# Performance work log

Hardware: AMD Instinct MI355X
Metric: run time of the kernel (lower is better)

Reference implementation:

```python
import jax, jax.numpy as jnp
import numpy as np

N_NODES = 50000
N_EDGES = 800000
F_IN = 128
HID = 32
H_IN = 4
N_CLS = 47
H_OUT = 4
NEG_SLOPE = 0.2


def _param(k, shape, scale=0.1):
    return jax.random.normal(k, shape, dtype=jnp.float32) * scale


def setup_inputs() -> dict:
    key = jax.random.key(0)
    ks = jax.random.split(key, 14)
    return {
        "x": jax.random.normal(ks[0], (N_NODES, F_IN), dtype=jnp.float32),
        "edge_index": jax.random.randint(ks[1], (2, N_EDGES), 0, N_NODES, dtype=jnp.int64),
        # layer 1: in -> hidden, heads_in, concat
        "W1": _param(ks[2], (F_IN, H_IN * HID)),
        "a1s": _param(ks[3], (H_IN, HID)),
        "a1d": _param(ks[4], (H_IN, HID)),
        "b1": _param(ks[5], (H_IN * HID,)),
        # layer 2: hidden*heads -> hidden, heads_in, concat
        "W2": _param(ks[6], (H_IN * HID, H_IN * HID)),
        "a2s": _param(ks[7], (H_IN, HID)),
        "a2d": _param(ks[8], (H_IN, HID)),
        "b2": _param(ks[9], (H_IN * HID,)),
        # layer 3: hidden*heads -> out, heads_out, mean (concat=False)
        "W3": _param(ks[10], (H_IN * HID, H_OUT * N_CLS)),
        "a3s": _param(ks[11], (H_OUT, N_CLS)),
        "a3d": _param(ks[12], (H_OUT, N_CLS)),
        "b3": _param(ks[13], (N_CLS,)),
    }


def gat_conv(x, W, att_src, att_dst, bias, src, dst, concat):
    """PyG GATConv (self-loops pre-appended in src/dst, eval mode)."""
    n = x.shape[0]
    H, C = att_src.shape
    h = (x @ W).reshape(n, H, C)                      # [N, H, C]
    a_src = jnp.sum(h * att_src[None], axis=-1)       # [N, H]
    a_dst = jnp.sum(h * att_dst[None], axis=-1)       # [N, H]
    alpha = a_src[src] + a_dst[dst]                   # [E, H]
    alpha = jnp.where(alpha >= 0, alpha, NEG_SLOPE * alpha)
    # segment softmax over destination nodes
    m = jax.ops.segment_max(alpha, dst, num_segments=n)  # [N, H]
    e = jnp.exp(alpha - m[dst])
    denom = jax.ops.segment_sum(e, dst, num_segments=n)  # [N, H]
    w = e / denom[dst]                                   # [E, H]
    msg = h[src] * w[:, :, None]                         # [E, H, C]
    out = jax.ops.segment_sum(msg, dst, num_segments=n)  # [N, H, C]
    if concat:
        out = out.reshape(n, H * C)
    else:
        out = out.mean(axis=1)
    return out + bias


def reference(x, edge_index, W1, a1s, a1d, b1, W2, a2s, a2d, b2, W3, a3s, a3d, b3):
    n = x.shape[0]
    loops = jnp.arange(n, dtype=edge_index.dtype)
    src = jnp.concatenate([edge_index[0], loops])
    dst = jnp.concatenate([edge_index[1], loops])
    h = gat_conv(x, W1, a1s, a1d, b1, src, dst, concat=True)
    h = jax.nn.relu(h)
    h = gat_conv(h, W2, a2s, a2d, b2, src, dst, concat=True)
    h = jax.nn.relu(h)
    h = gat_conv(h, W3, a3s, a3d, b3, src, dst, concat=False)
    return jax.nn.log_softmax(h, axis=1)
```

## Files before the change

kernel.cpp:

```cpp
#include <hip/hip_runtime.h>

typedef unsigned short u16;
typedef unsigned int uint32;
typedef __attribute__((ext_vector_type(8))) short short8;
typedef __attribute__((ext_vector_type(4))) float float4v;

#define N_NODES 50000
#define N_EDGES 800000
#define N_TOT   850000
#define NBH 256
#define NB_BKT ((N_NODES + 255) >> 8)
#define NODE_BLOCKS ((N_NODES + 3) / 4)

__device__ __forceinline__ float b2f(u16 u) {
  return __uint_as_float(((unsigned int)u) << 16);
}
__device__ __forceinline__ u16 f2b(float f) {
  unsigned int x = __float_as_uint(f);
  unsigned int r = (x + 0x7fffu + ((x >> 16) & 1u)) >> 16;
  return (u16)r;
}
__device__ __forceinline__ float lo_bf(uint32 g) { return __uint_as_float(g << 16); }
__device__ __forceinline__ float hi_bf(uint32 g) { return __uint_as_float(g & 0xffff0000u); }
__device__ __forceinline__ u16 conv_elem(const void* src, int i, int isf32) {
  if (isf32) return f2b(((const float*)src)[i]);
  return ((const u16*)src)[i];
}
__device__ __forceinline__ float lrelu(float a) { return (a >= 0.f) ? a : 0.2f * a; }
__device__ __forceinline__ int eget(const int* __restrict__ ei, int i, int isI64) {
  return isI64 ? ei[2 * i] : ei[i];
}

__global__ void reorder_all(const u16* __restrict__ x16,
                            const void* W1, const void* W2, const void* W3,
                            const void* a1s, const void* a1d, const void* b1,
                            const void* a2s, const void* a2d, const void* b2,
                            const void* a3s, const void* a3d, const void* b3,
                            int* __restrict__ flags,
                            u16* __restrict__ Wf1, u16* __restrict__ Wf2,
                            u16* __restrict__ Wf3, u16* __restrict__ wt) {
  __shared__ int shF;
  const int tid = threadIdx.x;
  if (tid == 0) shF = 0;
  __syncthreads();
  {
    int emax = 0;
    for (int i = tid; i < 4096; i += 256) {
      int e = (x16[i] >> 7) & 0xFF;
      emax = emax > e ? emax : e;
    }
    if (emax >= 140) atomicOr(&shF, 1);
  }
  __syncthreads();
  const int f32 = shF;
  if (blockIdx.x == 0 && tid == 0) flags[0] = f32;

  int idx = blockIdx.x * 256 + tid;
  if (idx < 57344) {
    const void* W; u16* Wf; int NCOLS, li;
    if (idx < 16384)      { W = W1; Wf = Wf1; NCOLS = 128; li = idx; }
    else if (idx < 32768) { W = W2; Wf = Wf2; NCOLS = 128; li = idx - 16384; }
    else                  { W = W3; Wf = Wf3; NCOLS = 188; li = idx - 32768; }
    int j = li & 7;
    int l = (li >> 3) & 63;
    int c = (li >> 9) & 3;
    int t = li >> 11;
    int k = c * 32 + (l >> 4) * 8 + j;
    int n = t * 16 + (l & 15);
    Wf[li] = (n < NCOLS) ? conv_elem(W, k * NCOLS + n, f32) : (u16)0;
  } else if (idx < 58535) {
    int li = idx - 57344;
    const void* src; int off;
    if (li < 128)       { src = a1s; off = 16384; }
    else if (li < 256)  { src = a1d; off = 16512; li -= 128; }
    else if (li < 384)  { src = b1;  off = 16640; li -= 256; }
    else if (li < 512)  { src = a2s; off = 33152; li -= 384; }
    else if (li < 640)  { src = a2d; off = 33280; li -= 512; }
    else if (li < 768)  { src = b2;  off = 33408; li -= 640; }
    else if (li < 956)  { src = a3s; off = 57600; li -= 768; }
    else if (li < 1144) { src = a3d; off = 57788; li -= 956; }
    else                { src = b3;  off = 57976; li -= 1144; }
    wt[off + li] = conv_elem(src, li, f32);
  }
}


__global__ __launch_bounds__(256) void pack_hist(const int* __restrict__ ei,
                                                 uint32* __restrict__ epack,
                                                 int* __restrict__ cnt) {
  __shared__ int hist[NB_BKT];
  __shared__ int shI;
  const int tid = threadIdx.x;
  if (tid == 0) shI = 0;
  for (int t = tid; t < NB_BKT; t += 256) hist[t] = 0;
  __syncthreads();
  if (ei[2 * tid + 1] != 0) atomicOr(&shI, 1);
  __syncthreads();
  const int i64 = shI ? 0 : 1;
  const int chunk = (N_EDGES + NBH - 1) / NBH;
  const int lo = blockIdx.x * chunk;
  const int hi = min(lo + chunk, N_EDGES);
  for (int e = lo + tid; e < hi; e += 256) {
    int s = eget(ei, e, i64);
    int d = eget(ei, N_EDGES + e, i64);
    epack[e] = ((uint32)d << 16) | (uint32)s;
    atomicAdd(&hist[d >> 8], 1);
  }
  __syncthreads();
  for (int t = tid; t < NB_BKT; t += 256) cnt[t * NBH + blockIdx.x] = hist[t];
}

__global__ __launch_bounds__(256) void scan_cols(int* __restrict__ cnt,
                                                 int* __restrict__ total) {
  __shared__ int ws[4];
  const int bkt = blockIdx.x;
  const int tid = threadIdx.x, lane = tid & 63, wv = tid >> 6;
  int v = cnt[bkt * NBH + tid];
  int incl = v;
#pragma unroll
  for (int off = 1; off < 64; off <<= 1) {
    int t = __shfl_up(incl, off, 64);
    if (lane >= off) incl += t;
  }
  if (lane == 63) ws[wv] = incl;
  __syncthreads();
  if (tid == 0) {
    int s = 0;
#pragma unroll
    for (int w = 0; w < 4; w++) { int t = ws[w]; ws[w] = s; s += t; }
    total[bkt] = s;
  }
  __syncthreads();
  cnt[bkt * NBH + tid] = ws[wv] + incl - v;
}

__global__ __launch_bounds__(256) void scatter_coarse(const uint32* __restrict__ epack,
                                                      const int* __restrict__ cnt,
                                                      const int* __restrict__ btotal,
                                                      uint32* __restrict__ staging) {
  __shared__ int shA[256];
  __shared__ int shW[4];
  const int tid = threadIdx.x, lane = tid & 63, wv = tid >> 6;
  {
    int v = (tid < NB_BKT) ? btotal[tid] : 0;
    int incl = v;
#pragma unroll
    for (int off = 1; off < 64; off <<= 1) {
      int t = __shfl_up(incl, off, 64);
      if (lane >= off) incl += t;
    }
    if (lane == 63) shW[wv] = incl;
    __syncthreads();
    if (tid == 0) {
      int s = 0;
#pragma unroll
      for (int w = 0; w < 4; w++) { int t = shW[w]; shW[w] = s; s += t; }
    }
    __syncthreads();
    shA[tid] = shW[wv] + incl - v;
  }
  __syncthreads();
  for (int t = tid; t < NB_BKT; t += 256) shA[t] += cnt[t * NBH + blockIdx.x];
  __syncthreads();
  const int chunk = (N_EDGES + NBH - 1) / NBH;
  const int lo = blockIdx.x * chunk;
  const int hi = min(lo + chunk, N_EDGES);
  for (int e = lo + tid; e < hi; e += 256) {
    uint32 pk = epack[e];
    int p = atomicAdd(&shA[pk >> 24], 1);
    staging[p] = pk;
  }
}

__global__ __launch_bounds__(256) void build_csr(const uint32* __restrict__ staging,
                                                 const int* __restrict__ btotal,
                                                 int* __restrict__ row_start,
                                                 u16* __restrict__ csr_dst,
                                                 int* __restrict__ csr_src32) {
  __shared__ int shA[256];
  __shared__ int shB[256];
  __shared__ int shW[4];
  const int b = blockIdx.x;
  const int tid = threadIdx.x;
  const int lane = tid & 63, wv = tid >> 6;
  {
    int v = (tid < NB_BKT) ? btotal[tid] : 0;
    int incl = v;
#pragma unroll
    for (int off = 1; off < 64; off <<= 1) {
      int t = __shfl_up(incl, off, 64);
      if (lane >= off) incl += t;
    }
    if (lane == 63) shW[wv] = incl;
    __syncthreads();
    if (tid == 0) {
      int s = 0;
#pragma unroll
      for (int w = 0; w < 4; w++) { int t = shW[w]; shW[w] = s; s += t; }
    }
    __syncthreads();
    shA[tid] = shW[wv] + incl - v;
  }
  __syncthreads();
  const int lo = shA[b];
  const int hi = lo + btotal[b];
  __syncthreads();
  shA[tid] = 0;
  __syncthreads();
  for (int i = lo + tid; i < hi; i += 256)
    atomicAdd(&shA[(staging[i] >> 16) & 255], 1);
  __syncthreads();
  int v = shA[tid];
  int incl = v;
#pragma unroll
  for (int off = 1; off < 64; off <<= 1) {
    int t = __shfl_up(incl, off, 64);
    if (lane >= off) incl += t;
  }
  if (lane == 63) shW[wv] = incl;
  __syncthreads();
  if (tid == 0) {
    int s = 0;
#pragma unroll
    for (int w = 0; w < 4; w++) { int t = shW[w]; shW[w] = s; s += t; }
  }
  __syncthreads();
  int excl = shW[wv] + incl - v;
  const int n = (b << 8) + tid;
  if (n < N_NODES) {
    int rs = lo + (b << 8) + excl + tid;
    row_start[n] = rs;
    csr_src32[rs] = n;
    u16 g16 = (u16)n;
    for (int k = 0; k <= v; k++) csr_dst[rs + k] = g16;
    shB[tid] = rs + 1;
  }
  if (b == NB_BKT - 1 && tid == 0) row_start[N_NODES] = N_TOT;
  __syncthreads();
  for (int i = lo + tid; i < hi; i += 256) {
    uint32 pk = staging[i];
    int p = atomicAdd(&shB[(pk >> 16) & 255], 1);
    csr_src32[p] = (int)(pk & 0xffffu);
  }
}

template <int NT, int NCOLS, int STRIDE, bool FUSE_A, bool CMAJOR, bool FUSE3, bool RAWX>
__global__ __launch_bounds__(256) void gemm_mfma(const void* __restrict__ X,
                                                 const u16* __restrict__ Wf,
                                                 const u16* __restrict__ attS,
                                                 const u16* __restrict__ attD,
                                                 const int* __restrict__ flags,
                                                 u16* __restrict__ H,
                                                 float* __restrict__ a_s,
                                                 float* __restrict__ a_d, int M) {
  const int wid = __builtin_amdgcn_readfirstlane(threadIdx.x >> 6);
  const int lane = threadIdx.x & 63;
  const int row0 = (blockIdx.x * 4 + wid) * 16;
  if (row0 >= M) return;
  const int qr = lane >> 4;
  const int ln = lane & 15;

  float4v acc[NT];
#pragma unroll
  for (int t = 0; t < NT; t++) acc[t] = (float4v){0.f, 0.f, 0.f, 0.f};

  const short8* Wf8 = (const short8*)Wf;
  const size_t aoff = (size_t)(row0 + ln) * 128 + qr * 8;
  int f32m = 0;
  if constexpr (RAWX) f32m = flags[0];

#pragma unroll
  for (int c = 0; c < 4; c++) {
    short8 afrag;
    if constexpr (RAWX) {
      if (f32m) {
        const float* ap = (const float*)X + aoff + c * 32;
        float4 lo = ((const float4*)ap)[0];
        float4 hi = ((const float4*)ap)[1];
        afrag[0] = (short)f2b(lo.x); afrag[1] = (short)f2b(lo.y);
        afrag[2] = (short)f2b(lo.z); afrag[3] = (short)f2b(lo.w);
        afrag[4] = (short)f2b(hi.x); afrag[5] = (short)f2b(hi.y);
        afrag[6] = (short)f2b(hi.z); afrag[7] = (short)f2b(hi.w);
      } else {
        afrag = *(const short8*)((const u16*)X + aoff + c * 32);
      }
    } else {
      afrag = *(const short8*)((const u16*)X + aoff + c * 32);
    }
#pragma unroll
    for (int t = 0; t < NT; t++) {
      short8 bfrag = Wf8[(t * 4 + c) * 64 + lane];
      acc[t] = __builtin_amdgcn_mfma_f32_16x16x32_bf16(afrag, bfrag, acc[t], 0, 0, 0);
    }
  }

#pragma unroll
  for (int t = 0; t < NT; t++) {
    int col = t * 16 + ln;
    if (col < NCOLS) {
      int off;
      if constexpr (CMAJOR) {
        int h = (col >= 141) ? 3 : (col >= 94) ? 2 : (col >= 47) ? 1 : 0;
        int c = col - h * 47;
        off = c * 4 + h;
      } else {
        off = col;
      }
#pragma unroll
      for (int i = 0; i < 4; i++) {
        H[(size_t)(row0 + qr * 4 + i) * STRIDE + off] = f2b(acc[t][i]);
      }
    } else {
      if constexpr (CMAJOR) {
#pragma unroll
        for (int i = 0; i < 4; i++) {
          H[(size_t)(row0 + qr * 4 + i) * STRIDE + col] = (u16)0x3F80;
        }
      }
    }
  }

  if constexpr (FUSE_A) {
    float aSf[NT], aDf[NT];
#pragma unroll
    for (int t = 0; t < NT; t++) {
      aSf[t] = b2f(attS[t * 16 + ln]);
      aDf[t] = b2f(attD[t * 16 + ln]);
    }
#pragma unroll
    for (int h = 0; h < 4; h++) {
#pragma unroll
      for (int i = 0; i < 4; i++) {
        float s = acc[2 * h][i] * aSf[2 * h] + acc[2 * h + 1][i] * aSf[2 * h + 1];
        float d = acc[2 * h][i] * aDf[2 * h] + acc[2 * h + 1][i] * aDf[2 * h + 1];
#pragma unroll
        for (int m = 1; m < 16; m <<= 1) {
          s += __shfl_xor(s, m, 64);
          d += __shfl_xor(d, m, 64);
        }
        if (ln == 0) {
          int r = row0 + qr * 4 + i;
          a_s[r * 4 + h] = s;
          a_d[r * 4 + h] = d;
        }
      }
    }
  }

  if constexpr (FUSE3) {
    float sh[4][4], dh[4][4];
#pragma unroll
    for (int h = 0; h < 4; h++)
#pragma unroll
      for (int i = 0; i < 4; i++) { sh[h][i] = 0.f; dh[h][i] = 0.f; }
#pragma unroll
    for (int t = 0; t < NT; t++) {
      int col = t * 16 + ln;
      bool v = (col < NCOLS);
      float aS = v ? b2f(attS[col]) : 0.f;
      float aD = v ? b2f(attD[col]) : 0.f;
      int hh = (col >= 141) ? 3 : (col >= 94) ? 2 : (col >= 47) ? 1 : 0;
      float aS0 = (hh == 0) ? aS : 0.f, aS1 = (hh == 1) ? aS : 0.f;
      float aS2 = (hh == 2) ? aS : 0.f, aS3 = (hh == 3) ? aS : 0.f;
      float aD0 = (hh == 0) ? aD : 0.f, aD1 = (hh == 1) ? aD : 0.f;
      float aD2 = (hh == 2) ? aD : 0.f, aD3 = (hh == 3) ? aD : 0.f;
#pragma unroll
      for (int i = 0; i < 4; i++) {
        float a = acc[t][i];
        sh[0][i] += a * aS0; sh[1][i] += a * aS1;
        sh[2][i] += a * aS2; sh[3][i] += a * aS3;
        dh[0][i] += a * aD0; dh[1][i] += a * aD1;
        dh[2][i] += a * aD2; dh[3][i] += a * aD3;
      }
    }
#pragma unroll
    for (int h = 0; h < 4; h++) {
#pragma unroll
      for (int i = 0; i < 4; i++) {
        float s = sh[h][i], d = dh[h][i];
#pragma unroll
        for (int m = 1; m < 16; m <<= 1) {
          s += __shfl_xor(s, m, 64);
          d += __shfl_xor(d, m, 64);
        }
        if (ln == 0) {
          int r = row0 + qr * 4 + i;
          a_s[r * 4 + h] = s;
          a_d[r * 4 + h] = d;
        }
      }
    }
  }
}

__global__ __launch_bounds__(256) void edge_weights(const int* __restrict__ csr_src,
                                                    const u16* __restrict__ csr_dst,
                                                    const float* __restrict__ a_s,
                                                    const float* __restrict__ a_d,
                                                    uint2* __restrict__ w, int nE) {
  int e = blockIdx.x * blockDim.x + threadIdx.x;
  if (e >= nE) return;
  int s = csr_src[e], d = csr_dst[e];
  float4 as = ((const float4*)a_s)[s];
  float4 ad = ((const float4*)a_d)[d];
  float w0 = __expf(lrelu(as.x + ad.x));
  float w1 = __expf(lrelu(as.y + ad.y));
  float w2 = __expf(lrelu(as.z + ad.z));
  float w3 = __expf(lrelu(as.w + ad.w));
  uint2 o;
  o.x = ((uint32)f2b(w1) << 16) | (uint32)f2b(w0);
  o.y = ((uint32)f2b(w3) << 16) | (uint32)f2b(w2);
  w[e] = o;
}


__global__ __launch_bounds__(256) void aggregate12(const u16* __restrict__ h,
                                                   const float* __restrict__ a_s,
                                                   const float* __restrict__ a_d,
                                                   const int* __restrict__ row_start,
                                                   const int* __restrict__ csr_src,
                                                   const u16* __restrict__ bias,
                                                   u16* __restrict__ out, int nN) {
  const int lane = threadIdx.x & 63;
  const int wid = __builtin_amdgcn_readfirstlane(threadIdx.x >> 6);
  const int n = blockIdx.x * 4 + wid;
  if (n >= nN) return;
  const int hL = lane >> 4;
  const uint32* h32 = (const uint32*)h;
  const float bias0 = b2f(bias[2 * lane]);
  const float bias1 = b2f(bias[2 * lane + 1]);
  const float adv = a_d[n * 4 + hL];
  int beg = row_start[n], end = row_start[n + 1];

  float acc0 = 0.f, acc1 = 0.f, den = 0.f;
  int e = beg;
  for (; e + 7 < end; e += 8) {
    int s[8];
    float av[8];
    uint32 g[8];
#pragma unroll
    for (int j = 0; j < 8; j++) s[j] = csr_src[e + j];
#pragma unroll
    for (int j = 0; j < 8; j++) av[j] = a_s[s[j] * 4 + hL];
#pragma unroll
    for (int j = 0; j < 8; j++) g[j] = h32[s[j] * 64 + lane];
#pragma unroll
    for (int j = 0; j < 8; j++) {
      float w = __expf(lrelu(av[j] + adv));
      den += w;
      acc0 += w * lo_bf(g[j]);
      acc1 += w * hi_bf(g[j]);
    }
  }
  for (; e + 3 < end; e += 4) {
    int s[4];
    float av[4];
    uint32 g[4];
#pragma unroll
    for (int j = 0; j < 4; j++) s[j] = csr_src[e + j];
#pragma unroll
    for (int j = 0; j < 4; j++) av[j] = a_s[s[j] * 4 + hL];
#pragma unroll
    for (int j = 0; j < 4; j++) g[j] = h32[s[j] * 64 + lane];
#pragma unroll
    for (int j = 0; j < 4; j++) {
      float w = __expf(lrelu(av[j] + adv));
      den += w;
      acc0 += w * lo_bf(g[j]);
      acc1 += w * hi_bf(g[j]);
    }
  }
  for (; e < end; ++e) {
    int s = csr_src[e];
    float w = __expf(lrelu(a_s[s * 4 + hL] + adv));
    uint32 g = h32[s * 64 + lane];
    den += w;
    acc0 += w * lo_bf(g);
    acc1 += w * hi_bf(g);
  }
  float inv = 1.0f / den;
  float o0 = fmaxf(acc0 * inv + bias0, 0.f);
  float o1 = fmaxf(acc1 * inv + bias1, 0.f);
  uint32 packed = ((uint32)f2b(o1) << 16) | (uint32)f2b(o0);
  ((uint32*)out)[n * 64 + lane] = packed;
}

__global__ __launch_bounds__(256) void aggregate3(const u16* __restrict__ h3,
                                                  const uint2* __restrict__ wbuf,
                                                  const int* __restrict__ row_start,
                                                  const int* __restrict__ csr_src,
                                                  const u16* __restrict__ b3,
                                                  const int* __restrict__ flags,
                                                  void* __restrict__ out, int nN) {
  const int lane = threadIdx.x & 63;
  const int wid = __builtin_amdgcn_readfirstlane(threadIdx.x >> 6);
  const int n = blockIdx.x * 4 + wid;
  if (n >= nN) return;
  const bool act = lane < 47;
  const int lidx = (lane <= 47) ? lane : 0;
  const float b3v = act ? b2f(b3[lane]) : 0.f;
  const int isf32 = flags[0];
  const uint2* h3v = (const uint2*)h3;
  int beg = row_start[n], end = row_start[n + 1];

  float acc0 = 0.f, acc1 = 0.f, acc2 = 0.f, acc3 = 0.f;
  int e = beg;
  for (; e + 7 < end; e += 8) {
    int s[8];
    uint2 wp[8];
    uint2 g[8];
#pragma unroll
    for (int j = 0; j < 8; j++) s[j] = csr_src[e + j];
#pragma unroll
    for (int j = 0; j < 8; j++) wp[j] = wbuf[e + j];
#pragma unroll
    for (int j = 0; j < 8; j++) g[j] = h3v[(size_t)s[j] * 48 + lidx];
#pragma unroll
    for (int j = 0; j < 8; j++) {
      float w0 = lo_bf(wp[j].x), w1 = hi_bf(wp[j].x);
      float w2 = lo_bf(wp[j].y), w3 = hi_bf(wp[j].y);
      acc0 += w0 * lo_bf(g[j].x);
      acc1 += w1 * hi_bf(g[j].x);
      acc2 += w2 * lo_bf(g[j].y);
      acc3 += w3 * hi_bf(g[j].y);
    }
  }
  for (; e + 3 < end; e += 4) {
    int s[4];
    uint2 wp[4];
    uint2 g[4];
#pragma unroll
    for (int j = 0; j < 4; j++) s[j] = csr_src[e + j];
#pragma unroll
    for (int j = 0; j < 4; j++) wp[j] = wbuf[e + j];
#pragma unroll
    for (int j = 0; j < 4; j++) g[j] = h3v[(size_t)s[j] * 48 + lidx];
#pragma unroll
    for (int j = 0; j < 4; j++) {
      float w0 = lo_bf(wp[j].x), w1 = hi_bf(wp[j].x);
      float w2 = lo_bf(wp[j].y), w3 = hi_bf(wp[j].y);
      acc0 += w0 * lo_bf(g[j].x);
      acc1 += w1 * hi_bf(g[j].x);
      acc2 += w2 * lo_bf(g[j].y);
      acc3 += w3 * hi_bf(g[j].y);
    }
  }
  for (; e < end; ++e) {
    int s = csr_src[e];
    uint2 wp = wbuf[e];
    uint2 g = h3v[(size_t)s * 48 + lidx];
    float w0 = lo_bf(wp.x), w1 = hi_bf(wp.x);
    float w2 = lo_bf(wp.y), w3 = hi_bf(wp.y);
    acc0 += w0 * lo_bf(g.x);
    acc1 += w1 * hi_bf(g.x);
    acc2 += w2 * lo_bf(g.y);
    acc3 += w3 * hi_bf(g.y);
  }
  float den0 = __shfl(acc0, 47, 64);
  float den1 = __shfl(acc1, 47, 64);
  float den2 = __shfl(acc2, 47, 64);
  float den3 = __shfl(acc3, 47, 64);
  float val = act ? 0.25f * (acc0 / den0 + acc1 / den1 + acc2 / den2 + acc3 / den3) + b3v
                  : -1e30f;
  float mx = val;
#pragma unroll
  for (int m = 1; m < 64; m <<= 1) mx = fmaxf(mx, __shfl_xor(mx, m, 64));
  float ex = act ? __expf(val - mx) : 0.f;
  float sm = ex;
#pragma unroll
  for (int m = 1; m < 64; m <<= 1) sm += __shfl_xor(sm, m, 64);
  float lse = mx + __logf(sm);
  if (act) {
    float r = val - lse;
    if (isf32) ((float*)out)[n * 47 + lane] = r;
    else       ((u16*)out)[n * 47 + lane] = f2b(r);
  }
}


extern "C" void kernel_launch(void* const* d_in, const int* in_sizes, int n_in,
                              void* d_out, int out_size, void* d_ws, size_t ws_size,
                              hipStream_t stream) {
  const void* x   = d_in[0];
  const void* ei  = d_in[1];
  const void* W1  = d_in[2];
  const void* a1s = d_in[3];
  const void* a1d = d_in[4];
  const void* b1  = d_in[5];
  const void* W2  = d_in[6];
  const void* a2s = d_in[7];
  const void* a2d = d_in[8];
  const void* b2  = d_in[9];
  const void* W3  = d_in[10];
  const void* a3s = d_in[11];
  const void* a3d = d_in[12];
  const void* b3  = d_in[13];
  const int* ei32 = (const int*)ei;

  auto au = [](size_t v) { return (v + 255) & ~(size_t)255; };
  char* p = (char*)d_ws;
  int* flags     = (int*)p; p += 256;
  u16* wt        = (u16*)p; p += au((size_t)58023 * 2);
  u16* Wf1       = (u16*)p; p += au((size_t)16384 * 2);
  u16* Wf2       = (u16*)p; p += au((size_t)16384 * 2);
  u16* Wf3       = (u16*)p; p += au((size_t)24576 * 2);
  int* row_start = (int*)p; p += au((size_t)(N_NODES + 1) * 4);
  int* cnt       = (int*)p; p += au((size_t)NB_BKT * NBH * 4);
  int* btotal    = (int*)p; p += au((size_t)NB_BKT * 4);
  int* csr_src32 = (int*)p; p += au((size_t)N_TOT * 4);
  u16* csr_dst   = (u16*)p; p += au((size_t)N_TOT * 2);
  uint2* wbuf    = (uint2*)p; p += au((size_t)N_TOT * 8);
  float* a_s     = (float*)p; p += au((size_t)N_NODES * 4 * 4);
  float* a_d     = (float*)p; p += au((size_t)N_NODES * 4 * 4);
  u16* hB        = (u16*)p; p += au((size_t)N_NODES * 128 * 2);
  u16* hA        = (u16*)p; p += au((size_t)N_NODES * 128 * 2);
  u16* h3        = (u16*)p; p += au((size_t)N_NODES * 192 * 2);
  uint32* epack   = (uint32*)h3;
  uint32* staging = (uint32*)(h3 + 1600000);

  const u16* a1sc = wt + 16384;
  const u16* a1dc = wt + 16512;
  const u16* b1c  = wt + 16640;
  const u16* a2sc = wt + 33152;
  const u16* a2dc = wt + 33280;
  const u16* b2c  = wt + 33408;
  const u16* a3sc = wt + 57600;
  const u16* a3dc = wt + 57788;
  const u16* b3c  = wt + 57976;

  const int gemmBlocks = (N_NODES / 16 + 3) / 4;
  const int edgeBlocks = (N_TOT + 255) / 256;

  pack_hist<<<NBH, 256, 0, stream>>>(ei32, epack, cnt);
  reorder_all<<<229, 256, 0, stream>>>((const u16*)x, W1, W2, W3, a1s, a1d, b1,
                                       a2s, a2d, b2, a3s, a3d, b3, flags,
                                       Wf1, Wf2, Wf3, wt);
  scan_cols<<<NB_BKT, 256, 0, stream>>>(cnt, btotal);
  scatter_coarse<<<NBH, 256, 0, stream>>>(epack, cnt, btotal, staging);
  build_csr<<<NB_BKT, 256, 0, stream>>>(staging, btotal, row_start, csr_dst, csr_src32);

  gemm_mfma<8, 128, 128, true, false, false, true><<<gemmBlocks, 256, 0, stream>>>(
      x, Wf1, a1sc, a1dc, flags, hA, a_s, a_d, N_NODES);
  aggregate12<<<NODE_BLOCKS, 256, 0, stream>>>(hA, a_s, a_d, row_start, csr_src32,
                                               b1c, hB, N_NODES);

  gemm_mfma<8, 128, 128, true, false, false, false><<<gemmBlocks, 256, 0, stream>>>(
      hB, Wf2, a2sc, a2dc, flags, hA, a_s, a_d, N_NODES);
  aggregate12<<<NODE_BLOCKS, 256, 0, stream>>>(hA, a_s, a_d, row_start, csr_src32,
                                               b2c, hB, N_NODES);

  gemm_mfma<12, 188, 192, false, true, true, false><<<gemmBlocks, 256, 0, stream>>>(
      hB, Wf3, a3sc, a3dc, flags, h3, a_s, a_d, N_NODES);
  edge_weights<<<edgeBlocks, 256, 0, stream>>>(csr_src32, csr_dst, a_s, a_d, wbuf, N_TOT);
  aggregate3<<<NODE_BLOCKS, 256, 0, stream>>>(h3, wbuf, row_start, csr_src32,
                                              b3c, flags, d_out, N_NODES);
}
```

Before: 303.8 us.

## Merge independent launches and precompute layer-3 attention projections in aggregation

Several independent kernels are merged into combined launches selected by block index: edge histogram with weight reorder, coarse scatter with the layer-1 GEMM, and the layer-3 GEMM with edge-weight computation. The layer-3 attention logits are now taken from W3·att vectors precomputed in the front kernel and applied inside the layer-2 aggregation epilogue, so edge weights no longer have to wait for the layer-3 GEMM. This is meant to cut launch count and serialization between stages. The cost is extra shuffle reductions in the aggregation and a small change in rounding, since the logits are computed from bf16 hidden values times fp32 projections rather than from the bf16 GEMM output.

Measured after the change: 306.8 us. No clear change (+1.0%).

```diff
diff --git a/kernel.cpp b/kernel.cpp
--- a/kernel.cpp
+++ b/kernel.cpp
@@ -11,6 +11,10 @@
 #define NBH 256
 #define NB_BKT ((N_NODES + 255) >> 8)
 #define NODE_BLOCKS ((N_NODES + 3) / 4)
+#define GEMM_BLOCKS ((N_NODES / 16 + 3) / 4)
+#define REORDER_ITEMS 59559
+#define REORDER_BLOCKS ((REORDER_ITEMS + 255) / 256)
+#define EDGE_BLOCKS ((N_TOT + 255) / 256)
 
 __device__ __forceinline__ float b2f(u16 u) {
   return __uint_as_float(((unsigned int)u) << 16);
@@ -31,83 +35,199 @@
   return isI64 ? ei[2 * i] : ei[i];
 }
 
-__global__ void reorder_all(const u16* __restrict__ x16,
-                            const void* W1, const void* W2, const void* W3,
-                            const void* a1s, const void* a1d, const void* b1,
-                            const void* a2s, const void* a2d, const void* b2,
-                            const void* a3s, const void* a3d, const void* b3,
-                            int* __restrict__ flags,
-                            u16* __restrict__ Wf1, u16* __restrict__ Wf2,
-                            u16* __restrict__ Wf3, u16* __restrict__ wt) {
-  __shared__ int shF;
+template <int NT, int NCOLS, int STRIDE, bool FUSE_A, bool CMAJOR, bool RAWX>
+__device__ __forceinline__ void gemm_body(int bid, const void* __restrict__ X,
+                                          const u16* __restrict__ Wf,
+                                          const u16* __restrict__ attS,
+                                          const u16* __restrict__ attD,
+                                          const int* __restrict__ flags,
+                                          u16* __restrict__ H,
+                                          float* __restrict__ a_s,
+                                          float* __restrict__ a_d, int M) {
+  const int wid = __builtin_amdgcn_readfirstlane(threadIdx.x >> 6);
+  const int lane = threadIdx.x & 63;
+  const int row0 = (bid * 4 + wid) * 16;
+  if (row0 >= M) return;
+  const int qr = lane >> 4;
+  const int ln = lane & 15;
+
+  float4v acc[NT];
+#pragma unroll
+  for (int t = 0; t < NT; t++) acc[t] = (float4v){0.f, 0.f, 0.f, 0.f};
+
+  const short8* Wf8 = (const short8*)Wf;
+  const size_t aoff = (size_t)(row0 + ln) * 128 + qr * 8;
+  int f32m = 0;
+  if constexpr (RAWX) f32m = flags[0];
+
+#pragma unroll
+  for (int c = 0; c < 4; c++) {
+    short8 afrag;
+    if constexpr (RAWX) {
+      if (f32m) {
+        const float* ap = (const float*)X + aoff + c * 32;
+        float4 lo = ((const float4*)ap)[0];
+        float4 hi = ((const float4*)ap)[1];
+        afrag[0] = (short)f2b(lo.x); afrag[1] = (short)f2b(lo.y);
+        afrag[2] = (short)f2b(lo.z); afrag[3] = (short)f2b(lo.w);
+        afrag[4] = (short)f2b(hi.x); afrag[5] = (short)f2b(hi.y);
+        afrag[6] = (short)f2b(hi.z); afrag[7] = (short)f2b(hi.w);
+      } else {
+        afrag = *(const short8*)((const u16*)X + aoff + c * 32);
+      }
+    } else {
+      afrag = *(const short8*)((const u16*)X + aoff + c * 32);
+    }
+#pragma unroll
+    for (int t = 0; t < NT; t++) {
+      short8 bfrag = Wf8[(t * 4 + c) * 64 + lane];
+      acc[t] = __builtin_amdgcn_mfma_f32_16x16x32_bf16(afrag, bfrag, acc[t], 0, 0, 0);
+    }
+  }
+
+#pragma unroll
+  for (int t = 0; t < NT; t++) {
+    int col = t * 16 + ln;
+    if (col < NCOLS) {
+      int off;
+      if constexpr (CMAJOR) {
+        int h = (col >= 141) ? 3 : (col >= 94) ? 2 : (col >= 47) ? 1 : 0;
+        int c = col - h * 47;
+        off = c * 4 + h;
+      } else {
+        off = col;
+      }
+#pragma unroll
+      for (int i = 0; i < 4; i++) {
+        H[(size_t)(row0 + qr * 4 + i) * STRIDE + off] = f2b(acc[t][i]);
+      }
+    } else {
+      if constexpr (CMAJOR) {
+#pragma unroll
+        for (int i = 0; i < 4; i++) {
+          H[(size_t)(row0 + qr * 4 + i) * STRIDE + col] = (u16)0x3F80;
+        }
+      }
+    }
+  }
+
+  if constexpr (FUSE_A) {
+    float aSf[NT], aDf[NT];
+#pragma unroll
+    for (int t = 0; t < NT; t++) {
+      aSf[t] = b2f(attS[t * 16 + ln]);
+      aDf[t] = b2f(attD[t * 16 + ln]);
+    }
+#pragma unroll
+    for (int h = 0; h < 4; h++) {
+#pragma unroll
+      for (int i = 0; i < 4; i++) {
+        float s = acc[2 * h][i] * aSf[2 * h] + acc[2 * h + 1][i] * aSf[2 * h + 1];
+        float d = acc[2 * h][i] * aDf[2 * h] + acc[2 * h + 1][i] * aDf[2 * h + 1];
+#pragma unroll
+        for (int m = 1; m < 16; m <<= 1) {
+          s += __shfl_xor(s, m, 64);
+          d += __shfl_xor(d, m, 64);
+        }
+        if (ln == 0) {
+          int r = row0 + qr * 4 + i;
+          a_s[r * 4 + h] = s;
+          a_d[r * 4 + h] = d;
+        }
+      }
+    }
+  }
+}
+
+__global__ __launch_bounds__(256) void front1(
+    const int* __restrict__ ei, const u16* __restrict__ x16,
+    const void* W1, const void* W2, const void* W3,
+    const void* a1s, const void* a1d, const void* b1,
+    const void* a2s, const void* a2d, const void* b2,
+    const void* a3s, const void* a3d, const void* b3,
+    int* __restrict__ flags,
+    u16* __restrict__ Wf1, u16* __restrict__ Wf2, u16* __restrict__ Wf3,
+    u16* __restrict__ wt, float* __restrict__ vs,
+    uint32* __restrict__ epack, int* __restrict__ cnt) {
   const int tid = threadIdx.x;
-  if (tid == 0) shF = 0;
-  __syncthreads();
-  {
-    int emax = 0;
-    for (int i = tid; i < 4096; i += 256) {
-      int e = (x16[i] >> 7) & 0xFF;
-      emax = emax > e ? emax : e;
-    }
-    if (emax >= 140) atomicOr(&shF, 1);
-  }
-  __syncthreads();
-  const int f32 = shF;
-  if (blockIdx.x == 0 && tid == 0) flags[0] = f32;
-
-  int idx = blockIdx.x * 256 + tid;
-  if (idx < 57344) {
-    const void* W; u16* Wf; int NCOLS, li;
-    if (idx < 16384)      { W = W1; Wf = Wf1; NCOLS = 128; li = idx; }
-    else if (idx < 32768) { W = W2; Wf = Wf2; NCOLS = 128; li = idx - 16384; }
-    else                  { W = W3; Wf = Wf3; NCOLS = 188; li = idx - 32768; }
-    int j = li & 7;
-    int l = (li >> 3) & 63;
-    int c = (li >> 9) & 3;
-    int t = li >> 11;
-    int k = c * 32 + (l >> 4) * 8 + j;
-    int n = t * 16 + (l & 15);
-    Wf[li] = (n < NCOLS) ? conv_elem(W, k * NCOLS + n, f32) : (u16)0;
-  } else if (idx < 58535) {
-    int li = idx - 57344;
-    const void* src; int off;
-    if (li < 128)       { src = a1s; off = 16384; }
-    else if (li < 256)  { src = a1d; off = 16512; li -= 128; }
-    else if (li < 384)  { src = b1;  off = 16640; li -= 256; }
-    else if (li < 512)  { src = a2s; off = 33152; li -= 384; }
-    else if (li < 640)  { src = a2d; off = 33280; li -= 512; }
-    else if (li < 768)  { src = b2;  off = 33408; li -= 640; }
-    else if (li < 956)  { src = a3s; off = 57600; li -= 768; }
-    else if (li < 1144) { src = a3d; off = 57788; li -= 956; }
-    else                { src = b3;  off = 57976; li -= 1144; }
-    wt[off + li] = conv_elem(src, li, f32);
-  }
-}
-
-
-__global__ __launch_bounds__(256) void pack_hist(const int* __restrict__ ei,
-                                                 uint32* __restrict__ epack,
-                                                 int* __restrict__ cnt) {
-  __shared__ int hist[NB_BKT];
-  __shared__ int shI;
-  const int tid = threadIdx.x;
-  if (tid == 0) shI = 0;
-  for (int t = tid; t < NB_BKT; t += 256) hist[t] = 0;
-  __syncthreads();
-  if (ei[2 * tid + 1] != 0) atomicOr(&shI, 1);
-  __syncthreads();
-  const int i64 = shI ? 0 : 1;
-  const int chunk = (N_EDGES + NBH - 1) / NBH;
-  const int lo = blockIdx.x * chunk;
-  const int hi = min(lo + chunk, N_EDGES);
-  for (int e = lo + tid; e < hi; e += 256) {
-    int s = eget(ei, e, i64);
-    int d = eget(ei, N_EDGES + e, i64);
-    epack[e] = ((uint32)d << 16) | (uint32)s;
-    atomicAdd(&hist[d >> 8], 1);
-  }
-  __syncthreads();
-  for (int t = tid; t < NB_BKT; t += 256) cnt[t * NBH + blockIdx.x] = hist[t];
+  if (blockIdx.x < NBH) {
+    __shared__ int hist[NB_BKT];
+    __shared__ int shI;
+    if (tid == 0) shI = 0;
+    for (int t = tid; t < NB_BKT; t += 256) hist[t] = 0;
+    __syncthreads();
+    if (ei[2 * tid + 1] != 0) atomicOr(&shI, 1);
+    __syncthreads();
+    const int i64 = shI ? 0 : 1;
+    const int chunk = (N_EDGES + NBH - 1) / NBH;
+    const int lo = blockIdx.x * chunk;
+    const int hi = min(lo + chunk, N_EDGES);
+    for (int e = lo + tid; e < hi; e += 256) {
+      int s = eget(ei, e, i64);
+      int d = eget(ei, N_EDGES + e, i64);
+      epack[e] = ((uint32)d << 16) | (uint32)s;
+      atomicAdd(&hist[d >> 8], 1);
+    }
+    __syncthreads();
+    for (int t = tid; t < NB_BKT; t += 256) cnt[t * NBH + blockIdx.x] = hist[t];
+  } else {
+    __shared__ int shF;
+    if (tid == 0) shF = 0;
+    __syncthreads();
+    {
+      int emax = 0;
+      for (int i = tid; i < 4096; i += 256) {
+        int e = (x16[i] >> 7) & 0xFF;
+        emax = emax > e ? emax : e;
+      }
+      if (emax >= 140) atomicOr(&shF, 1);
+    }
+    __syncthreads();
+    const int f32 = shF;
+    const int bid2 = blockIdx.x - NBH;
+    if (bid2 == 0 && tid == 0) flags[0] = f32;
+
+    int idx = bid2 * 256 + tid;
+    if (idx < 57344) {
+      const void* W; u16* Wf; int NCOLS, li;
+      if (idx < 16384)      { W = W1; Wf = Wf1; NCOLS = 128; li = idx; }
+      else if (idx < 32768) { W = W2; Wf = Wf2; NCOLS = 128; li = idx - 16384; }
+      else                  { W = W3; Wf = Wf3; NCOLS = 188; li = idx - 32768; }
+      int j = li & 7;
+      int l = (li >> 3) & 63;
+      int c = (li >> 9) & 3;
+      int t = li >> 11;
+      int k = c * 32 + (l >> 4) * 8 + j;
+      int n = t * 16 + (l & 15);
+      Wf[li] = (n < NCOLS) ? conv_elem(W, k * NCOLS + n, f32) : (u16)0;
+    } else if (idx < 58535) {
+      int li = idx - 57344;
+      const void* src; int off;
+      if (li < 128)       { src = a1s; off = 16384; }
+      else if (li < 256)  { src = a1d; off = 16512; li -= 128; }
+      else if (li < 384)  { src = b1;  off = 16640; li -= 256; }
+      else if (li < 512)  { src = a2s; off = 33152; li -= 384; }
+      else if (li < 640)  { src = a2d; off = 33280; li -= 512; }
+      else if (li < 768)  { src = b2;  off = 33408; li -= 640; }
+      else if (li < 956)  { src = a3s; off = 57600; li -= 768; }
+      else if (li < 1144) { src = a3d; off = 57788; li -= 956; }
+      else                { src = b3;  off = 57976; li -= 1144; }
+      wt[off + li] = conv_elem(src, li, f32);
+    } else if (idx < REORDER_ITEMS) {
+      int li = idx - 58535;
+      const void* att = (li < 512) ? a3s : a3d;
+      int hh = (li >> 7) & 3;
+      int k = li & 127;
+      int base = hh * 47;
+      float sum = 0.f;
+      for (int c = 0; c < 47; c++) {
+        float wv = b2f(conv_elem(W3, k * 188 + base + c, f32));
+        float av = b2f(conv_elem(att, base + c, f32));
+        sum += wv * av;
+      }
+      vs[li] = sum;
+    }
+  }
 }
 
 __global__ __launch_bounds__(256) void scan_cols(int* __restrict__ cnt,
@@ -134,41 +254,50 @@
   cnt[bkt * NBH + tid] = ws[wv] + incl - v;
 }
 
-__global__ __launch_bounds__(256) void scatter_coarse(const uint32* __restrict__ epack,
-                                                      const int* __restrict__ cnt,
-                                                      const int* __restrict__ btotal,
-                                                      uint32* __restrict__ staging) {
-  __shared__ int shA[256];
-  __shared__ int shW[4];
-  const int tid = threadIdx.x, lane = tid & 63, wv = tid >> 6;
-  {
-    int v = (tid < NB_BKT) ? btotal[tid] : 0;
-    int incl = v;
-#pragma unroll
-    for (int off = 1; off < 64; off <<= 1) {
-      int t = __shfl_up(incl, off, 64);
-      if (lane >= off) incl += t;
-    }
-    if (lane == 63) shW[wv] = incl;
-    __syncthreads();
-    if (tid == 0) {
-      int s = 0;
-#pragma unroll
-      for (int w = 0; w < 4; w++) { int t = shW[w]; shW[w] = s; s += t; }
-    }
-    __syncthreads();
-    shA[tid] = shW[wv] + incl - v;
-  }
-  __syncthreads();
-  for (int t = tid; t < NB_BKT; t += 256) shA[t] += cnt[t * NBH + blockIdx.x];
-  __syncthreads();
-  const int chunk = (N_EDGES + NBH - 1) / NBH;
-  const int lo = blockIdx.x * chunk;
-  const int hi = min(lo + chunk, N_EDGES);
-  for (int e = lo + tid; e < hi; e += 256) {
-    uint32 pk = epack[e];
-    int p = atomicAdd(&shA[pk >> 24], 1);
-    staging[p] = pk;
+__global__ __launch_bounds__(256) void front2(
+    const uint32* __restrict__ epack, const int* __restrict__ cnt,
+    const int* __restrict__ btotal, uint32* __restrict__ staging,
+    const void* __restrict__ X, const u16* __restrict__ Wf1,
+    const u16* __restrict__ attS, const u16* __restrict__ attD,
+    const int* __restrict__ flags, u16* __restrict__ H,
+    float* __restrict__ a_s, float* __restrict__ a_d) {
+  const int tid = threadIdx.x;
+  if (blockIdx.x < NBH) {
+    __shared__ int shA[256];
+    __shared__ int shW[4];
+    const int lane = tid & 63, wv = tid >> 6;
+    {
+      int v = (tid < NB_BKT) ? btotal[tid] : 0;
+      int incl = v;
+#pragma unroll
+      for (int off = 1; off < 64; off <<= 1) {
+        int t = __shfl_up(incl, off, 64);
+        if (lane >= off) incl += t;
+      }
+      if (lane == 63) shW[wv] = incl;
+      __syncthreads();
+      if (tid == 0) {
+        int s = 0;
+#pragma unroll
+        for (int w = 0; w < 4; w++) { int t = shW[w]; shW[w] = s; s += t; }
+      }
+      __syncthreads();
+      shA[tid] = shW[wv] + incl - v;
+    }
+    __syncthreads();
+    for (int t = tid; t < NB_BKT; t += 256) shA[t] += cnt[t * NBH + blockIdx.x];
+    __syncthreads();
+    const int chunk = (N_EDGES + NBH - 1) / NBH;
+    const int lo = blockIdx.x * chunk;
+    const int hi = min(lo + chunk, N_EDGES);
+    for (int e = lo + tid; e < hi; e += 256) {
+      uint32 pk = epack[e];
+      int p = atomicAdd(&shA[pk >> 24], 1);
+      staging[p] = pk;
+    }
+  } else {
+    gemm_body<8, 128, 128, true, false, true>(blockIdx.x - NBH, X, Wf1, attS, attD,
+                                              flags, H, a_s, a_d, N_NODES);
   }
 }
 
@@ -244,183 +373,56 @@
   }
 }
 
-template <int NT, int NCOLS, int STRIDE, bool FUSE_A, bool CMAJOR, bool FUSE3, bool RAWX>
-__global__ __launch_bounds__(256) void gemm_mfma(const void* __restrict__ X,
-                                                 const u16* __restrict__ Wf,
-                                                 const u16* __restrict__ attS,
-                                                 const u16* __restrict__ attD,
-                                                 const int* __restrict__ flags,
-                                                 u16* __restrict__ H,
-                                                 float* __restrict__ a_s,
-                                                 float* __restrict__ a_d, int M) {
-  const int wid = __builtin_amdgcn_readfirstlane(threadIdx.x >> 6);
-  const int lane = threadIdx.x & 63;
-  const int row0 = (blockIdx.x * 4 + wid) * 16;
-  if (row0 >= M) return;
-  const int qr = lane >> 4;
-  const int ln = lane & 15;
-
-  float4v acc[NT];
-#pragma unroll
-  for (int t = 0; t < NT; t++) acc[t] = (float4v){0.f, 0.f, 0.f, 0.f};
-
-  const short8* Wf8 = (const short8*)Wf;
-  const size_t aoff = (size_t)(row0 + ln) * 128 + qr * 8;
-  int f32m = 0;
-  if constexpr (RAWX) f32m = flags[0];
-
-#pragma unroll
-  for (int c = 0; c < 4; c++) {
-    short8 afrag;
-    if constexpr (RAWX) {
-      if (f32m) {
-        const float* ap = (const float*)X + aoff + c * 32;
-        float4 lo = ((const float4*)ap)[0];
-        float4 hi = ((const float4*)ap)[1];
-        afrag[0] = (short)f2b(lo.x); afrag[1] = (short)f2b(lo.y);
-        afrag[2] = (short)f2b(lo.z); afrag[3] = (short)f2b(lo.w);
-        afrag[4] = (short)f2b(hi.x); afrag[5] = (short)f2b(hi.y);
-        afrag[6] = (short)f2b(hi.z); afrag[7] = (short)f2b(hi.w);
-      } else {
-        afrag = *(const short8*)((const u16*)X + aoff + c * 32);
-      }
-    } else {
-      afrag = *(const short8*)((const u16*)X + aoff + c * 32);
-    }
-#pragma unroll
-    for (int t = 0; t < NT; t++) {
-      short8 bfrag = Wf8[(t * 4 + c) * 64 + lane];
-      acc[t] = __builtin_amdgcn_mfma_f32_16x16x32_bf16(afrag, bfrag, acc[t], 0, 0, 0);
-    }
-  }
-
-#pragma unroll
-  for (int t = 0; t < NT; t++) {
-    int col = t * 16 + ln;
-    if (col < NCOLS) {
-      int off;
-      if constexpr (CMAJOR) {
-        int h = (col >= 141) ? 3 : (col >= 94) ? 2 : (col >= 47) ? 1 : 0;
-        int c = col - h * 47;
-        off = c * 4 + h;
-      } else {
-        off = col;
-      }
-#pragma unroll
-      for (int i = 0; i < 4; i++) {
-        H[(size_t)(row0 + qr * 4 + i) * STRIDE + off] = f2b(acc[t][i]);
-      }
-    } else {
-      if constexpr (CMAJOR) {
-#pragma unroll
-        for (int i = 0; i < 4; i++) {
-          H[(size_t)(row0 + qr * 4 + i) * STRIDE + col] = (u16)0x3F80;
-        }
-      }
-    }
-  }
-
-  if constexpr (FUSE_A) {
-    float aSf[NT], aDf[NT];
-#pragma unroll
-    for (int t = 0; t < NT; t++) {
-      aSf[t] = b2f(attS[t * 16 + ln]);
-      aDf[t] = b2f(attD[t * 16 + ln]);
-    }
-#pragma unroll
-    for (int h = 0; h < 4; h++) {
-#pragma unroll
-      for (int i = 0; i < 4; i++) {
-        float s = acc[2 * h][i] * aSf[2 * h] + acc[2 * h + 1][i] * aSf[2 * h + 1];
-        float d = acc[2 * h][i] * aDf[2 * h] + acc[2 * h + 1][i] * aDf[2 * h + 1];
-#pragma unroll
-        for (int m = 1; m < 16; m <<= 1) {
-          s += __shfl_xor(s, m, 64);
-          d += __shfl_xor(d, m, 64);
-        }
-        if (ln == 0) {
-          int r = row0 + qr * 4 + i;
-          a_s[r * 4 + h] = s;
-          a_d[r * 4 + h] = d;
-        }
-      }
-    }
-  }
-
-  if constexpr (FUSE3) {
-    float sh[4][4], dh[4][4];
-#pragma unroll
-    for (int h = 0; h < 4; h++)
-#pragma unroll
-      for (int i = 0; i < 4; i++) { sh[h][i] = 0.f; dh[h][i] = 0.f; }
-#pragma unroll
-    for (int t = 0; t < NT; t++) {
-      int col = t * 16 + ln;
-      bool v = (col < NCOLS);
-      float aS = v ? b2f(attS[col]) : 0.f;
-      float aD = v ? b2f(attD[col]) : 0.f;
-      int hh = (col >= 141) ? 3 : (col >= 94) ? 2 : (col >= 47) ? 1 : 0;
-      float aS0 = (hh == 0) ? aS : 0.f, aS1 = (hh == 1) ? aS : 0.f;
-      float aS2 = (hh == 2) ? aS : 0.f, aS3 = (hh == 3) ? aS : 0.f;
-      float aD0 = (hh == 0) ? aD : 0.f, aD1 = (hh == 1) ? aD : 0.f;
-      float aD2 = (hh == 2) ? aD : 0.f, aD3 = (hh == 3) ? aD : 0.f;
-#pragma unroll
-      for (int i = 0; i < 4; i++) {
-        float a = acc[t][i];
-        sh[0][i] += a * aS0; sh[1][i] += a * aS1;
-        sh[2][i] += a * aS2; sh[3][i] += a * aS3;
-        dh[0][i] += a * aD0; dh[1][i] += a * aD1;
-        dh[2][i] += a * aD2; dh[3][i] += a * aD3;
-      }
-    }
-#pragma unroll
-    for (int h = 0; h < 4; h++) {
-#pragma unroll
-      for (int i = 0; i < 4; i++) {
-        float s = sh[h][i], d = dh[h][i];
-#pragma unroll
-        for (int m = 1; m < 16; m <<= 1) {
-          s += __shfl_xor(s, m, 64);
-          d += __shfl_xor(d, m, 64);
-        }
-        if (ln == 0) {
-          int r = row0 + qr * 4 + i;
-          a_s[r * 4 + h] = s;
-          a_d[r * 4 + h] = d;
-        }
-      }
-    }
-  }
-}
-
-__global__ __launch_bounds__(256) void edge_weights(const int* __restrict__ csr_src,
-                                                    const u16* __restrict__ csr_dst,
-                                                    const float* __restrict__ a_s,
-                                                    const float* __restrict__ a_d,
-                                                    uint2* __restrict__ w, int nE) {
-  int e = blockIdx.x * blockDim.x + threadIdx.x;
-  if (e >= nE) return;
-  int s = csr_src[e], d = csr_dst[e];
-  float4 as = ((const float4*)a_s)[s];
-  float4 ad = ((const float4*)a_d)[d];
-  float w0 = __expf(lrelu(as.x + ad.x));
-  float w1 = __expf(lrelu(as.y + ad.y));
-  float w2 = __expf(lrelu(as.z + ad.z));
-  float w3 = __expf(lrelu(as.w + ad.w));
-  uint2 o;
-  o.x = ((uint32)f2b(w1) << 16) | (uint32)f2b(w0);
-  o.y = ((uint32)f2b(w3) << 16) | (uint32)f2b(w2);
-  w[e] = o;
-}
-
-
+__global__ __launch_bounds__(256) void gemm2_k(const void* __restrict__ X,
+                                               const u16* __restrict__ Wf,
+                                               const u16* __restrict__ attS,
+                                               const u16* __restrict__ attD,
+                                               const int* __restrict__ flags,
+                                               u16* __restrict__ H,
+                                               float* __restrict__ a_s,
+                                               float* __restrict__ a_d) {
+  gemm_body<8, 128, 128, true, false, false>(blockIdx.x, X, Wf, attS, attD, flags,
+                                             H, a_s, a_d, N_NODES);
+}
+
+__global__ __launch_bounds__(256) void fused3(
+    const void* __restrict__ X, const u16* __restrict__ Wf3,
+    const int* __restrict__ flags, u16* __restrict__ H,
+    const int* __restrict__ csr_src, const u16* __restrict__ csr_dst,
+    const float* __restrict__ a_s3, const float* __restrict__ a_d3,
+    uint2* __restrict__ w) {
+  if (blockIdx.x < GEMM_BLOCKS) {
+    gemm_body<12, 188, 192, false, true, false>(blockIdx.x, X, Wf3, nullptr, nullptr,
+                                                flags, H, nullptr, nullptr, N_NODES);
+  } else {
+    int e = (blockIdx.x - GEMM_BLOCKS) * 256 + threadIdx.x;
+    if (e >= N_TOT) return;
+    int s = csr_src[e], d = csr_dst[e];
+    float4 as = ((const float4*)a_s3)[s];
+    float4 ad = ((const float4*)a_d3)[d];
+    float w0 = __expf(lrelu(as.x + ad.x));
+    float w1 = __expf(lrelu(as.y + ad.y));
+    float w2 = __expf(lrelu(as.z + ad.z));
+    float w3 = __expf(lrelu(as.w + ad.w));
+    uint2 o;
+    o.x = ((uint32)f2b(w1) << 16) | (uint32)f2b(w0);
+    o.y = ((uint32)f2b(w3) << 16) | (uint32)f2b(w2);
+    w[e] = o;
+  }
+}
+
+
+template <bool A3>
 __global__ __launch_bounds__(256) void aggregate12(const u16* __restrict__ h,
                                                    const float* __restrict__ a_s,
                                                    const float* __restrict__ a_d,
                                                    const int* __restrict__ row_start,
                                                    const int* __restrict__ csr_src,
                                                    const u16* __restrict__ bias,
-                                                   u16* __restrict__ out, int nN) {
+                                                   u16* __restrict__ out,
+                                                   const float* __restrict__ vs,
+                                                   float* __restrict__ a_s3,
+                                                   float* __restrict__ a_d3, int nN) {
   const int lane = threadIdx.x & 63;
   const int wid = __builtin_amdgcn_readfirstlane(threadIdx.x >> 6);
   const int n = blockIdx.x * 4 + wid;
@@ -481,8 +483,36 @@
   float inv = 1.0f / den;
   float o0 = fmaxf(acc0 * inv + bias0, 0.f);
   float o1 = fmaxf(acc1 * inv + bias1, 0.f);
-  uint32 packed = ((uint32)f2b(o1) << 16) | (uint32)f2b(o0);
+  u16 r0 = f2b(o0), r1 = f2b(o1);
+  uint32 packed = ((uint32)r1 << 16) | (uint32)r0;
   ((uint32*)out)[n * 64 + lane] = packed;
+
+  if constexpr (A3) {
+    float o0r = b2f(r0), o1r = b2f(r1);
+    const float* vsS = vs;
+    const float* vsD = vs + 512;
+    float ps[4], pd[4];
+#pragma unroll
+    for (int hh = 0; hh < 4; hh++) {
+      ps[hh] = o0r * vsS[hh * 128 + 2 * lane] + o1r * vsS[hh * 128 + 2 * lane + 1];
+      pd[hh] = o0r * vsD[hh * 128 + 2 * lane] + o1r * vsD[hh * 128 + 2 * lane + 1];
+    }
+#pragma unroll
+    for (int m = 1; m < 64; m <<= 1) {
+#pragma unroll
+      for (int hh = 0; hh < 4; hh++) {
+        ps[hh] += __shfl_xor(ps[hh], m, 64);
+        pd[hh] += __shfl_xor(pd[hh], m, 64);
+      }
+    }
+    if (lane == 0) {
+#pragma unroll
+      for (int hh = 0; hh < 4; hh++) {
+        a_s3[n * 4 + hh] = ps[hh];
+        a_d3[n * 4 + hh] = pd[hh];
+      }
+    }
+  }
 }
 
 __global__ __launch_bounds__(256) void aggregate3(const u16* __restrict__ h3,
@@ -601,6 +631,7 @@
   char* p = (char*)d_ws;
   int* flags     = (int*)p; p += 256;
   u16* wt        = (u16*)p; p += au((size_t)58023 * 2);
+  float* vs      = (float*)p; p += au((size_t)1024 * 4);
   u16* Wf1       = (u16*)p; p += au((size_t)16384 * 2);
   u16* Wf2       = (u16*)p; p += au((size_t)16384 * 2);
   u16* Wf3       = (u16*)p; p += au((size_t)24576 * 2);
@@ -612,6 +643,8 @@
   uint2* wbuf    = (uint2*)p; p += au((size_t)N_TOT * 8);
   float* a_s     = (float*)p; p += au((size_t)N_NODES * 4 * 4);
   float* a_d     = (float*)p; p += au((size_t)N_NODES * 4 * 4);
+  float* a_s3    = (float*)p; p += au((size_t)N_NODES * 4 * 4);
+  float* a_d3    = (float*)p; p += au((size_t)N_NODES * 4 * 4);
   u16* hB        = (u16*)p; p += au((size_t)N_NODES * 128 * 2);
   u16* hA        = (u16*)p; p += au((size_t)N_NODES * 128 * 2);
   u16* h3        = (u16*)p; p += au((size_t)N_NODES * 192 * 2);
@@ -624,34 +657,30 @@
   const u16* a2sc = wt + 33152;
   const u16* a2dc = wt + 33280;
   const u16* b2c  = wt + 33408;
-  const u16* a3sc = wt + 57600;
-  const u16* a3dc = wt + 57788;
   const u16* b3c  = wt + 57976;
 
-  const int gemmBlocks = (N_NODES / 16 + 3) / 4;
-  const int edgeBlocks = (N_TOT + 255) / 256;
-
-  pack_hist<<<NBH, 256, 0, stream>>>(ei32, epack, cnt);
-  reorder_all<<<229, 256, 0, stream>>>((const u16*)x, W1, W2, W3, a1s, a1d, b1,
-                                       a2s, a2d, b2, a3s, a3d, b3, flags,
-                                       Wf1, Wf2, Wf3, wt);
+  front1<<<NBH + REORDER_BLOCKS, 256, 0, stream>>>(
+      ei32, (const u16*)x, W1, W2, W3, a1s, a1d, b1, a2s, a2d, b2, a3s, a3d, b3,
+      flags, Wf1, Wf2, Wf3, wt, vs, epack, cnt);
   scan_cols<<<NB_BKT, 256, 0, stream>>>(cnt, btotal);
-  scatter_coarse<<<NBH, 256, 0, stream>>>(epack, cnt, btotal, staging);
+  front2<<<NBH + GEMM_BLOCKS, 256, 0, stream>>>(epack, cnt, btotal, staging,
+                                                x, Wf1, a1sc, a1dc, flags,
+                                                hA, a_s, a_d);
   build_csr<<<NB_BKT, 256, 0, stream>>>(staging, btotal, row_start, csr_dst, csr_src32);
 
-  gemm_mfma<8, 128, 128, true, false, false, true><<<gemmBlocks, 256, 0, stream>>>(
-      x, Wf1, a1sc, a1dc, flags, hA, a_s, a_d, N_NODES);
-  aggregate12<<<NODE_BLOCKS, 256, 0, stream>>>(hA, a_s, a_d, row_start, csr_src32,
-                                               b1c, hB, N_NODES);
-
-  gemm_mfma<8, 128, 128, true, false, false, false><<<gemmBlocks, 256, 0, stream>>>(
-      hB, Wf2, a2sc, a2dc, flags, hA, a_s, a_d, N_NODES);
-  aggregate12<<<NODE_BLOCKS, 256, 0, stream>>>(hA, a_s, a_d, row_start, csr_src32,
-                                               b2c, hB, N_NODES);
-
-  gemm_mfma<12, 188, 192, false, true, true, false><<<gemmBlocks, 256, 0, stream>>>(
-      hB, Wf3, a3sc, a3dc, flags, h3, a_s, a_d, N_NODES);
-  edge_weights<<<edgeBlocks, 256, 0, stream>>>(csr_src32, csr_dst, a_s, a_d, wbuf, N_TOT);
+  aggregate12<false><<<NODE_BLOCKS, 256, 0, stream>>>(hA, a_s, a_d, row_start,
+                                                      csr_src32, b1c, hB,
+                                                      nullptr, nullptr, nullptr,
+                                                      N_NODES);
+
+  gemm2_k<<<GEMM_BLOCKS, 256, 0, stream>>>(hB, Wf2, a2sc, a2dc, flags, hA, a_s, a_d);
+  aggregate12<true><<<NODE_BLOCKS, 256, 0, stream>>>(hA, a_s, a_d, row_start,
+                                                     csr_src32, b2c, hB,
+                                                     vs, a_s3, a_d3, N_NODES);
+
+  fused3<<<GEMM_BLOCKS + EDGE_BLOCKS, 256, 0, stream>>>(hB, Wf3, flags, h3,
+                                                        csr_src32, csr_dst,
+                                                        a_s3, a_d3, wbuf);
   aggregate3<<<NODE_BLOCKS, 256, 0, stream>>>(h3, wbuf, row_start, csr_src32,
                                               b3c, flags, d_out, N_NODES);
 }
```
